# Kernel optimization log

Measured on AMD Instinct MI355X. Metric: run time of the kernel, lower is better.

Reference implementation:

```python
import jax, jax.numpy as jnp
import numpy as np

N, E, F, H, G, C = 50000, 800000, 128, 128, 500, 10
L = 3  # num_conv_layers
EPS = 1e-5


def batch_norm(x, g, b):
    # training-mode BatchNorm1d: biased variance, eps=1e-5
    mu = jnp.mean(x, axis=0)
    var = jnp.var(x, axis=0)
    return (x - mu) * jax.lax.rsqrt(var + EPS) * g + b


def gcn_conv(x, W, bias, src, dst, n):
    # x' = D^{-1/2} (A + I) D^{-1/2} (x W) + bias, edge weights = 1
    xw = x @ W
    loop = jnp.arange(n)
    s = jnp.concatenate([src, loop])  # sources incl. self-loops
    d = jnp.concatenate([dst, loop])  # targets incl. self-loops
    w = jnp.ones(s.shape[0], x.dtype)
    deg = jax.ops.segment_sum(w, s, num_segments=n)
    dinv = jnp.where(deg > 0, jax.lax.rsqrt(deg), 0.0)
    norm = dinv[s] * w * dinv[d]
    msg = xw[s] * norm[:, None]  # gather + scale
    out = jax.ops.segment_sum(msg, d, num_segments=n)  # scatter-add
    return out + bias


def setup_inputs() -> dict:
    key = jax.random.key(0)
    ks = jax.random.split(key, 16)
    x = jax.random.normal(ks[0], (N, F), dtype=jnp.float32)
    edge_index = jax.random.randint(ks[1], (2, E), 0, N, dtype=jnp.int64)
    batch = jnp.sort(jax.random.randint(ks[2], (N,), 0, G, dtype=jnp.int64))
    sF = 1.0 / np.sqrt(F)
    sH = 1.0 / np.sqrt(H)
    return {
        "x": x,
        "edge_index": edge_index,
        "batch": batch,
        "bn_feat_g": jnp.ones((F,), jnp.float32),
        "bn_feat_b": jnp.full((F,), 1e-4, jnp.float32),
        "W_feat": jax.random.normal(ks[3], (F, H), jnp.float32) * sF,
        "bns_conv_g": jnp.ones((L, H), jnp.float32),
        "bns_conv_b": jnp.full((L, H), 1e-4, jnp.float32),
        "W_conv": jax.random.normal(ks[4], (L, H, H), jnp.float32) * sH,
        "b_conv": jnp.zeros((L, H), jnp.float32),
        "bn_fc_g": jnp.ones((H,), jnp.float32),
        "bn_fc_b": jnp.full((H,), 1e-4, jnp.float32),
        "W_lin": jax.random.normal(ks[5], (H, H), jnp.float32) * sH,
        "b_lin": jnp.zeros((H,), jnp.float32),
        "bn_hid_g": jnp.ones((H,), jnp.float32),
        "bn_hid_b": jnp.full((H,), 1e-4, jnp.float32),
        "W_cls": jax.random.normal(ks[6], (H, C), jnp.float32) * sH,
        "b_cls": jnp.zeros((C,), jnp.float32),
    }


def reference(x, edge_index, batch, bn_feat_g, bn_feat_b, W_feat,
              bns_conv_g, bns_conv_b, W_conv, b_conv,
              bn_fc_g, bn_fc_b, W_lin, b_lin,
              bn_hid_g, bn_hid_b, W_cls, b_cls):
    src, dst = edge_index[0], edge_index[1]
    h = batch_norm(x, bn_feat_g, bn_feat_b)
    h = jax.nn.relu(h @ W_feat)  # gfn conv: linear only, no bias/propagation
    for i in range(L):
        h = batch_norm(h, bns_conv_g[i], bns_conv_b[i])
        h = jax.nn.relu(gcn_conv(h, W_conv[i], b_conv[i], src, dst, N))
    h = jax.ops.segment_sum(h, batch, num_segments=G)  # global_add_pool
    h = batch_norm(h, bn_fc_g, bn_fc_b)
    h = jax.nn.relu(h @ W_lin + b_lin)
    h = batch_norm(h, bn_hid_g, bn_hid_b)
    logits = h @ W_cls + b_cls
    return jax.nn.log_softmax(logits, axis=-1)
```

## Files before the change

kernel.cpp:

```cpp
#include <hip/hip_runtime.h>

#define NF 128
#define EPS 1e-5f
#define KELL 64
#define HB 64
#define HRANGE 32768
#define BCAP 5120

typedef unsigned short ushort_t;
typedef unsigned int uint_t;

using bf16x8 = __attribute__((ext_vector_type(8))) short;
using f32x4  = __attribute__((ext_vector_type(4))) float;
using f32x2  = __attribute__((ext_vector_type(2))) float;

static __device__ inline ushort_t f2bf(float f) {
    uint_t u = __float_as_uint(f);
    return (ushort_t)((u + 0x7fffu + ((u >> 16) & 1u)) >> 16);
}


__launch_bounds__(1024)
__global__ void k_bucket(const int* __restrict__ ei, uint_t* __restrict__ gcnt,
                         uint_t* __restrict__ bedge, int E) {
    __shared__ uint_t cnt[256];
    __shared__ uint_t cur[256];
    __shared__ uint_t base[256];
    const int t = threadIdx.x;
    if (t < 256) { cnt[t] = 0; cur[t] = 0; }
    __syncthreads();
    const int chunk = (E + gridDim.x - 1) / gridDim.x;
    const int e0 = blockIdx.x * chunk;
    const int e1 = min(e0 + chunk, E);
    for (int e = e0 + t; e < e1; e += 1024)
        atomicAdd(&cnt[ei[E + e] >> 8], 1);
    __syncthreads();
    if (t < 256) {
        uint_t c = cnt[t];
        base[t] = c ? atomicAdd(&gcnt[t], c) : 0u;
    }
    __syncthreads();
    for (int e = e0 + t; e < e1; e += 1024) {
        int s = ei[e], d = ei[E + e];
        int b = d >> 8;
        uint_t pos = base[b] + atomicAdd(&cur[b], 1);
        if (pos < BCAP)
            bedge[((size_t)b << 12) + ((size_t)b << 10) + pos] =
                ((uint_t)(d & 255) << 16) | (uint_t)s;
    }
}

__global__ void k_hist(const int* __restrict__ ei, uint_t* __restrict__ partial, int E) {
    __shared__ uint_t h2[HRANGE / 2];
    int b = blockIdx.x, t = threadIdx.x;
#pragma unroll
    for (int p = 0; p < 2; ++p) {
        int base = p * HRANGE;
        for (int w = t; w < HRANGE / 2; w += 256) h2[w] = 0;
        __syncthreads();
        for (int e = b * 256 + t; e < E; e += HB * 256) {
            unsigned u = (unsigned)(ei[e] - base);
            if (u < HRANGE)
                atomicAdd(&h2[u >> 1], 1u << ((u & 1) << 4));
        }
        __syncthreads();
        uint_t* dst = partial + ((size_t)(p * HB + b) << 14);
        for (int w = t; w < HRANGE / 2; w += 256) dst[w] = h2[w];
        __syncthreads();
    }
}

__launch_bounds__(256)
__global__ void k_build(const uint_t* __restrict__ gcnt, const uint_t* __restrict__ bedge,
                        const uint_t* __restrict__ hpart, int* __restrict__ ucnt,
                        float* __restrict__ dinv, ushort_t* __restrict__ colx,
                        ushort_t* __restrict__ BbSent, int n) {
    __shared__ ushort_t ell[256][KELL];
    __shared__ uint_t lcnt[256];
    const int b = blockIdx.x, t = threadIdx.x;
    lcnt[t] = 0;
    __syncthreads();
    const int nb = min((int)gcnt[b], BCAP);
    const int node0 = b << 8;
    const uint_t* bsrc = bedge + ((size_t)b << 12) + ((size_t)b << 10);
    for (int e = t; e < nb; e += 256) {
        uint_t pk = bsrc[e];
        int dl = (pk >> 16) & 255;
        uint_t pos = atomicAdd(&lcnt[dl], 1);
        if (pos < KELL - 1) ell[dl][pos] = (ushort_t)(pk & 0xffffu);
    }
    __syncthreads();
    const int i = node0 + t;
    if (i < n) {
        int w = min((int)lcnt[t], KELL - 1);
        ell[t][w] = (ushort_t)i;
        int len = (w + 16) & ~15;
        for (int q = w + 1; q < len; ++q) ell[t][q] = (ushort_t)n;
        ucnt[i] = w;
        int p = i >> 15;
        int u = i & (HRANGE - 1);
        int wd = u >> 1, sh = (u & 1) << 4;
        const uint_t* basep = hpart + ((size_t)(p * HB) << 14) + wd;
        uint_t sum = 0;
#pragma unroll 8
        for (int bb = 0; bb < HB; ++bb) sum += basep[(size_t)bb << 14];
        sum = (sum >> sh) & 0xffffu;
        dinv[i] = rsqrtf((float)sum + 1.0f);
    }
    __syncthreads();
    int nrow = min(n - node0, 256);
    if (nrow > 0) {
        const uint4* src = (const uint4*)&ell[0][0];
        uint4* dst = (uint4*)&colx[(size_t)node0 * KELL];
        int lim = nrow * (KELL * 2 / 16);
        for (int wds = t; wds < lim; wds += 256) dst[wds] = src[wds];
    }
    if (b == 0 && t < 64)
        ((uint_t*)BbSent)[t] = 0;
}


__global__ void bn_stats(const float* __restrict__ h, float* __restrict__ stats, int n) {
    int j = threadIdx.x & 127;
    int half = threadIdx.x >> 7;
    float s = 0.f, q = 0.f;
    for (int r = blockIdx.x * 2 + half; r < n; r += gridDim.x * 2) {
        float v = h[r * NF + j];
        s += v;
        q += v * v;
    }
    __shared__ float ls[256], lq[256];
    ls[threadIdx.x] = s; lq[threadIdx.x] = q;
    __syncthreads();
    if (threadIdx.x < 128) {
        atomicAdd(&stats[j], ls[threadIdx.x] + ls[threadIdx.x + 128]);
        atomicAdd(&stats[NF + j], lq[threadIdx.x] + lq[threadIdx.x + 128]);
    }
}


__global__ void pack_w4(const float* __restrict__ W0, const float* __restrict__ W123,
                        ushort_t* __restrict__ Wp) {
    int gidx = blockIdx.x * 256 + threadIdx.x;
    int mat = gidx >> 11, idx = gidx & 2047;
    const float* W = (mat == 0) ? W0 : (W123 + (size_t)(mat - 1) * NF * NF);
    int lane = idx & 63, ct = (idx >> 6) & 7, kc = idx >> 9;
    int m = lane & 15, q = lane >> 4;
    ushort_t o[8];
#pragma unroll
    for (int j = 0; j < 8; ++j)
        o[j] = f2bf(W[(kc * 32 + q * 8 + j) * NF + ct * 16 + m]);
    *(uint4*)&Wp[(size_t)gidx * 8] = *(uint4*)o;
}


#define HSTRIDE 136

__launch_bounds__(256)
__global__ void gemm_mfma(const float* __restrict__ Hh, const ushort_t* __restrict__ Wp,
                          const float* __restrict__ stats, const float* __restrict__ gW,
                          const float* __restrict__ bB, float inv_n,
                          const float* __restrict__ bias, const float* __restrict__ rowscale,
                          float* __restrict__ out, ushort_t* __restrict__ outb,
                          int nrows, int relu, int obf) {
    __shared__ ushort_t hs[64 * HSTRIDE];
    __shared__ float acs[256];
    const int tid = threadIdx.x;
    const int rb = blockIdx.x * 64;

    if (tid < 128) {
        float mean = stats[tid] * inv_n;
        float var = stats[NF + tid] * inv_n - mean * mean;
        float rstd = rsqrtf(var + EPS);
        float a = gW[tid] * rstd;
        acs[tid] = a;
        acs[NF + tid] = bB[tid] - mean * a;
    }
    __syncthreads();
    const float4* ac4 = (const float4*)acs;

#pragma unroll
    for (int p = 0; p < 8; ++p) {
        int idx = p * 256 + tid;
        int r = idx >> 5, k4 = idx & 31;
        int gr = rb + r;
        float4 v = (gr < nrows) ? *(const float4*)&Hh[(size_t)gr * NF + k4 * 4]
                                : make_float4(0.f, 0.f, 0.f, 0.f);
        float4 a4 = ac4[k4], c4 = ac4[32 + k4];
        ushort_t o[4];
        o[0] = f2bf(fmaf(v.x, a4.x, c4.x));
        o[1] = f2bf(fmaf(v.y, a4.y, c4.y));
        o[2] = f2bf(fmaf(v.z, a4.z, c4.z));
        o[3] = f2bf(fmaf(v.w, a4.w, c4.w));
        *(uint2*)&hs[r * HSTRIDE + k4 * 4] = *(uint2*)o;
    }
    __syncthreads();

    const int wave = tid >> 6, lane = tid & 63;
    const int m = lane & 15, q = lane >> 4;
    const ushort_t* arow = &hs[(wave * 16 + m) * HSTRIDE];

    f32x4 acc[8];
#pragma unroll
    for (int ct = 0; ct < 8; ++ct) acc[ct] = (f32x4){0.f, 0.f, 0.f, 0.f};

#pragma unroll
    for (int kc = 0; kc < 4; ++kc) {
        bf16x8 af = *(const bf16x8*)&arow[kc * 32 + q * 8];
        const ushort_t* wp = Wp + kc * 4096 + lane * 8;
#pragma unroll
        for (int ct = 0; ct < 8; ++ct) {
            bf16x8 bfr = *(const bf16x8*)&wp[ct * 512];
            acc[ct] = __builtin_amdgcn_mfma_f32_16x16x32_bf16(af, bfr, acc[ct], 0, 0, 0);
        }
    }

#pragma unroll
    for (int r = 0; r < 4; ++r) {
        int grow = rb + wave * 16 + q * 4 + r;
        if (grow < nrows) {
            float rs = (obf && rowscale) ? rowscale[grow] : 1.0f;
#pragma unroll
            for (int ct = 0; ct < 8; ++ct) {
                int col = ct * 16 + m;
                float v = acc[ct][r] + (bias ? bias[col] : 0.f);
                if (relu) v = fmaxf(v, 0.f);
                if (obf) outb[(size_t)grow * NF + col] = f2bf(v * rs);
                else     out[(size_t)grow * NF + col] = v;
            }
        }
    }
}


__launch_bounds__(256)
__global__ void gemm_bn(const float* __restrict__ Hh, const float* __restrict__ W,
                        const float* __restrict__ stats, const float* __restrict__ gW,
                        const float* __restrict__ bB, float inv_n,
                        const float* __restrict__ bias,
                        float* __restrict__ out, int nrows, int relu) {
    __shared__ float hsb[64][133];
    __shared__ float acs[256];
    const int tid = threadIdx.x;
    const int tx = tid & 15;
    const int ty = tid >> 4;
    const int rb = blockIdx.x * 64;

    if (tid < 128) {
        float mean = stats[tid] * inv_n;
        float var = stats[NF + tid] * inv_n - mean * mean;
        float rstd = rsqrtf(var + EPS);
        float a = gW[tid] * rstd;
        acs[tid] = a;
        acs[NF + tid] = bB[tid] - mean * a;
    }
    __syncthreads();

#pragma unroll 8
    for (int p = 0; p < 32; ++p) {
        int idx = p * 256 + tid;
        int r = idx >> 7, k = idx & 127;
        int gr = rb + r;
        float v = (gr < nrows) ? Hh[(size_t)gr * NF + k] : 0.f;
        hsb[r][k] = fmaf(v, acs[k], acs[NF + k]);
    }
    __syncthreads();

    float acc[4][8];
#pragma unroll
    for (int i = 0; i < 4; ++i)
#pragma unroll
        for (int j = 0; j < 8; ++j) acc[i][j] = 0.f;

    const int c0 = tx * 4, c1 = 64 + tx * 4;
#pragma unroll 4
    for (int k = 0; k < 128; ++k) {
        const float4 b0 = *(const float4*)&W[k * NF + c0];
        const float4 b1 = *(const float4*)&W[k * NF + c1];
#pragma unroll
        for (int i = 0; i < 4; ++i) {
            float a = hsb[ty * 4 + i][k];
            acc[i][0] = fmaf(a, b0.x, acc[i][0]);
            acc[i][1] = fmaf(a, b0.y, acc[i][1]);
            acc[i][2] = fmaf(a, b0.z, acc[i][2]);
            acc[i][3] = fmaf(a, b0.w, acc[i][3]);
            acc[i][4] = fmaf(a, b1.x, acc[i][4]);
            acc[i][5] = fmaf(a, b1.y, acc[i][5]);
            acc[i][6] = fmaf(a, b1.z, acc[i][6]);
            acc[i][7] = fmaf(a, b1.w, acc[i][7]);
        }
    }

#pragma unroll
    for (int i = 0; i < 4; ++i) {
        int gr = rb + ty * 4 + i;
        if (gr < nrows) {
            float o[8];
#pragma unroll
            for (int j = 0; j < 8; ++j) {
                int c = (j < 4) ? (c0 + j) : (c1 + j - 4);
                float v = acc[i][j] + (bias ? bias[c] : 0.f);
                o[j] = relu ? fmaxf(v, 0.f) : v;
            }
            *(float4*)&out[(size_t)gr * NF + c0] = make_float4(o[0], o[1], o[2], o[3]);
            *(float4*)&out[(size_t)gr * NF + c1] = make_float4(o[4], o[5], o[6], o[7]);
        }
    }
}


#define ACC2(u, j) { f32x2 t;                                   \
    t.x = __uint_as_float((u) << 16);                           \
    t.y = __uint_as_float((u) & 0xffff0000u);                   \
    acc2[j] += t; }
#define ACC8(q) { ACC2(q.x, 0) ACC2(q.y, 1) ACC2(q.z, 2) ACC2(q.w, 3) }

__launch_bounds__(256)
__global__ void k_aggregate_bf(const ushort_t* __restrict__ xwb, const int* __restrict__ ucnt,
                               const ushort_t* __restrict__ colx, const float* __restrict__ dinv,
                               const float* __restrict__ bias, float* __restrict__ out, int n) {
    int node = blockIdx.x * 16 + (threadIdx.x >> 4);
    int lane = threadIdx.x & 15;
    if (node >= n) return;
    const uint4* __restrict__ xq = (const uint4*)xwb;
    f32x2 acc2[4];
#pragma unroll
    for (int j = 0; j < 4; ++j) acc2[j] = (f32x2){0.f, 0.f};
    int dc = min(ucnt[node], KELL - 1);
    int len = (dc + 16) & ~15;
    int e0 = node * KELL;
    for (int e = e0; e < e0 + len; e += 16) {
        uint4 ia = *(const uint4*)&colx[e];
        uint4 ib = *(const uint4*)&colx[e + 8];
        int i0 = ia.x & 0xffff, i1 = ia.x >> 16;
        int i2 = ia.y & 0xffff, i3 = ia.y >> 16;
        int i4 = ia.z & 0xffff, i5 = ia.z >> 16;
        int i6 = ia.w & 0xffff, i7 = ia.w >> 16;
        int i8 = ib.x & 0xffff, i9 = ib.x >> 16;
        int iA = ib.y & 0xffff, iB = ib.y >> 16;
        int iC = ib.z & 0xffff, iD = ib.z >> 16;
        int iE = ib.w & 0xffff, iF = ib.w >> 16;
        uint4 q0 = xq[(size_t)i0 * 16 + lane];
        uint4 q1 = xq[(size_t)i1 * 16 + lane];
        uint4 q2 = xq[(size_t)i2 * 16 + lane];
        uint4 q3 = xq[(size_t)i3 * 16 + lane];
        uint4 q4 = xq[(size_t)i4 * 16 + lane];
        uint4 q5 = xq[(size_t)i5 * 16 + lane];
        uint4 q6 = xq[(size_t)i6 * 16 + lane];
        uint4 q7 = xq[(size_t)i7 * 16 + lane];
        uint4 q8 = xq[(size_t)i8 * 16 + lane];
        uint4 q9 = xq[(size_t)i9 * 16 + lane];
        uint4 qA = xq[(size_t)iA * 16 + lane];
        uint4 qB = xq[(size_t)iB * 16 + lane];
        uint4 qC = xq[(size_t)iC * 16 + lane];
        uint4 qD = xq[(size_t)iD * 16 + lane];
        uint4 qE = xq[(size_t)iE * 16 + lane];
        uint4 qF = xq[(size_t)iF * 16 + lane];
        ACC8(q0) ACC8(q1) ACC8(q2) ACC8(q3)
        ACC8(q4) ACC8(q5) ACC8(q6) ACC8(q7)
        ACC8(q8) ACC8(q9) ACC8(qA) ACC8(qB)
        ACC8(qC) ACC8(qD) ACC8(qE) ACC8(qF)
    }
    float di = dinv[node];
    float4 b0 = *(const float4*)&bias[lane * 8];
    float4 b1 = *(const float4*)&bias[lane * 8 + 4];
    float4 o0, o1;
    o0.x = fmaxf(fmaf(di, acc2[0].x, b0.x), 0.f);
    o0.y = fmaxf(fmaf(di, acc2[0].y, b0.y), 0.f);
    o0.z = fmaxf(fmaf(di, acc2[1].x, b0.z), 0.f);
    o0.w = fmaxf(fmaf(di, acc2[1].y, b0.w), 0.f);
    o1.x = fmaxf(fmaf(di, acc2[2].x, b1.x), 0.f);
    o1.y = fmaxf(fmaf(di, acc2[2].y, b1.y), 0.f);
    o1.z = fmaxf(fmaf(di, acc2[3].x, b1.z), 0.f);
    o1.w = fmaxf(fmaf(di, acc2[3].y, b1.w), 0.f);
    *(float4*)&out[(size_t)node * NF + lane * 8] = o0;
    *(float4*)&out[(size_t)node * NF + lane * 8 + 4] = o1;
}


__global__ void k_pool(const float* __restrict__ h, const int* __restrict__ batch,
                       float* __restrict__ pooled, float* __restrict__ stats, int n) {
    int g = blockIdx.x;
    int t = threadIdx.x;
    int lo = 0, hi = n;
    while (lo < hi) { int m = (lo + hi) >> 1; if (batch[m] < g) lo = m + 1; else hi = m; }
    int start = lo;
    lo = start; hi = n;
    while (lo < hi) { int m = (lo + hi) >> 1; if (batch[m] < g + 1) lo = m + 1; else hi = m; }
    int end = lo;
    float a0 = 0.f, a1 = 0.f, a2 = 0.f, a3 = 0.f;
    int r = start;
    for (; r + 4 <= end; r += 4) {
        a0 += h[(size_t)r * NF + t];
        a1 += h[(size_t)(r + 1) * NF + t];
        a2 += h[(size_t)(r + 2) * NF + t];
        a3 += h[(size_t)(r + 3) * NF + t];
    }
    for (; r < end; ++r) a0 += h[(size_t)r * NF + t];
    float val = (a0 + a1) + (a2 + a3);
    pooled[g * NF + t] = val;
    atomicAdd(&stats[t], val);
    atomicAdd(&stats[NF + t], val * val);
}


__global__ void k_cls(const float* __restrict__ h, const float* __restrict__ stats,
                      const float* __restrict__ gW, const float* __restrict__ bB,
                      float inv_n, const float* __restrict__ Wc,
                      const float* __restrict__ bc, float* __restrict__ out, int C_) {
    __shared__ float hr[128];
    __shared__ float lg[16];
    __shared__ float lse_s;
    int r = blockIdx.x, t = threadIdx.x;
#pragma unroll
    for (int half = 0; half < 2; ++half) {
        int j = t + half * 64;
        float mean = stats[j] * inv_n;
        float var = stats[NF + j] * inv_n - mean * mean;
        float rstd = rsqrtf(var + EPS);
        float a = gW[j] * rstd;
        float c = bB[j] - mean * a;
        hr[j] = fmaf(h[r * NF + j], a, c);
    }
    __syncthreads();
    if (t < C_) {
        float s = bc[t];
        for (int k = 0; k < 128; ++k) s = fmaf(hr[k], Wc[k * C_ + t], s);
        lg[t] = s;
    }
    __syncthreads();
    if (t == 0) {
        float m = -1e30f;
        for (int c = 0; c < C_; ++c) m = fmaxf(m, lg[c]);
        float se = 0.f;
        for (int c = 0; c < C_; ++c) se += expf(lg[c] - m);
        lse_s = m + logf(se);
    }
    __syncthreads();
    if (t < C_) out[r * C_ + t] = lg[t] - lse_s;
}


extern "C" void kernel_launch(void* const* d_in, const int* in_sizes, int n_in,
                              void* d_out, int out_size, void* d_ws, size_t ws_size,
                              hipStream_t stream) {
    const float* x          = (const float*)d_in[0];
    const int*   ei         = (const int*)d_in[1];
    const int*   batch      = (const int*)d_in[2];
    const float* bn_feat_g  = (const float*)d_in[3];
    const float* bn_feat_b  = (const float*)d_in[4];
    const float* W_feat     = (const float*)d_in[5];
    const float* bns_conv_g = (const float*)d_in[6];
    const float* bns_conv_b = (const float*)d_in[7];
    const float* W_conv     = (const float*)d_in[8];
    const float* b_conv     = (const float*)d_in[9];
    const float* bn_fc_g    = (const float*)d_in[10];
    const float* bn_fc_b    = (const float*)d_in[11];
    const float* W_lin      = (const float*)d_in[12];
    const float* b_lin      = (const float*)d_in[13];
    const float* bn_hid_g   = (const float*)d_in[14];
    const float* bn_hid_b   = (const float*)d_in[15];
    const float* W_cls      = (const float*)d_in[16];
    const float* b_cls      = (const float*)d_in[17];
    float* outp = (float*)d_out;

    const int N_ = in_sizes[2];
    const int E_ = in_sizes[1] / 2;
    const int C_ = 10;
    const int G_ = out_size / C_;
    const int NBUCK = (N_ + 255) >> 8;

    char* wsp = (char*)d_ws;
    auto alloc = [&](size_t bytes) {
        void* p = (void*)wsp;
        wsp += (bytes + 255) & ~(size_t)255;
        return p;
    };
    uint_t*   gcnt   = (uint_t*)alloc(256 * 4);
    float*    statsA = (float*)alloc(6 * 256 * 4);
    float*    A      = (float*)alloc((size_t)N_ * NF * 4);
    ushort_t* Bb     = (ushort_t*)alloc((size_t)(N_ + 1) * NF * 2);
    float*    dinv   = (float*)alloc((size_t)N_ * 4);
    int*      ucnt   = (int*)alloc((size_t)N_ * 4);
    uint_t*   bedge  = (uint_t*)alloc((size_t)256 * BCAP * 4);
    ushort_t* colx   = (ushort_t*)alloc((size_t)N_ * KELL * 2);
    uint_t*   hpart  = (uint_t*)alloc((size_t)2 * HB * (HRANGE / 2) * 4);
    ushort_t* Wp     = (ushort_t*)alloc((size_t)4 * NF * NF * 2);
    float*    pooled = (float*)alloc((size_t)G_ * NF * 4);
    float*    y2     = (float*)alloc((size_t)G_ * NF * 4);

    float* st_x  = statsA;
    float* st_f  = statsA + 256;
    float* st_a1 = statsA + 512;
    float* st_a2 = statsA + 768;
    float* st_pl = statsA + 1024;
    float* st_y2 = statsA + 1280;

    int nb_g = (N_ + 63) / 64;

    hipMemsetAsync(gcnt, 0, 1024 + 6 * 256 * 4, stream);

    k_bucket<<<256, 1024, 0, stream>>>(ei, gcnt, bedge, E_);
    k_hist<<<HB, 256, 0, stream>>>(ei, hpart, E_);
    k_build<<<NBUCK, 256, 0, stream>>>(gcnt, bedge, hpart, ucnt, dinv, colx,
                                       Bb + (size_t)N_ * NF, N_);

    pack_w4<<<32, 256, 0, stream>>>(W_feat, W_conv, Wp);

    bn_stats<<<512, 256, 0, stream>>>(x, st_x, N_);
    gemm_mfma<<<nb_g, 256, 0, stream>>>(x, Wp, st_x, bn_feat_g, bn_feat_b, 1.0f / N_,
                                        nullptr, nullptr, A, nullptr, N_, 1, 0);
    bn_stats<<<512, 256, 0, stream>>>(A, st_f, N_);

    float* st_in[3] = {st_f, st_a1, st_a2};
    float* st_out[3] = {st_a1, st_a2, nullptr};
    for (int l = 0; l < 3; ++l) {
        gemm_mfma<<<nb_g, 256, 0, stream>>>(A, Wp + (size_t)(l + 1) * NF * NF,
                                            st_in[l], bns_conv_g + l * NF, bns_conv_b + l * NF,
                                            1.0f / N_, nullptr, dinv, nullptr, Bb, N_, 0, 1);
        k_aggregate_bf<<<(N_ + 15) / 16, 256, 0, stream>>>(Bb, ucnt, colx, dinv,
                                                           b_conv + l * NF, A, N_);
        if (st_out[l])
            bn_stats<<<512, 256, 0, stream>>>(A, st_out[l], N_);
    }

    k_pool<<<G_, 128, 0, stream>>>(A, batch, pooled, st_pl, N_);

    gemm_bn<<<(G_ + 63) / 64, 256, 0, stream>>>(pooled, W_lin, st_pl, bn_fc_g, bn_fc_b,
                                                1.0f / G_, b_lin, y2, G_, 1);
    bn_stats<<<512, 256, 0, stream>>>(y2, st_y2, G_);

    k_cls<<<G_, 64, 0, stream>>>(y2, st_y2, bn_hid_g, bn_hid_b, 1.0f / G_,
                                 W_cls, b_cls, outp, C_);
}
```

Measured before the change: 479.3 us.

## Fuse BN statistics into GEMM/aggregate epilogues and merge prep kernels

Computes the column sum and sum-of-squares for batch norm inside the epilogues of the GEMM, aggregation and small GEMM kernels, which removes four separate bn_stats passes over the activations. The bucket, histogram and weight-packing kernels become one launch split by block index. The ELL padding granularity drops from 16 to 8 entries, which cuts wasted gathers, and the aggregate kernel now uses 1024-thread blocks. In exchange it adds shared and global atomics plus block syncs in the epilogues, and the per-thread float accumulation order changes.

Result: no change. 486.0 us (+1.4%).

```diff
diff --git a/kernel.cpp b/kernel.cpp
--- a/kernel.cpp
+++ b/kernel.cpp
@@ -21,52 +21,70 @@
 
 
 __launch_bounds__(1024)
-__global__ void k_bucket(const int* __restrict__ ei, uint_t* __restrict__ gcnt,
-                         uint_t* __restrict__ bedge, int E) {
-    __shared__ uint_t cnt[256];
-    __shared__ uint_t cur[256];
-    __shared__ uint_t base[256];
+__global__ void k_prep(const int* __restrict__ ei, uint_t* __restrict__ gcnt,
+                       uint_t* __restrict__ bedge, uint_t* __restrict__ hpart,
+                       const float* __restrict__ W0, const float* __restrict__ W123,
+                       ushort_t* __restrict__ Wp, int E) {
+    __shared__ union {
+        struct { uint_t cnt[256]; uint_t cur[256]; uint_t base[256]; } bk;
+        uint_t h2[HRANGE / 2];
+    } sh;
+    const int blk = blockIdx.x;
     const int t = threadIdx.x;
-    if (t < 256) { cnt[t] = 0; cur[t] = 0; }
-    __syncthreads();
-    const int chunk = (E + gridDim.x - 1) / gridDim.x;
-    const int e0 = blockIdx.x * chunk;
-    const int e1 = min(e0 + chunk, E);
-    for (int e = e0 + t; e < e1; e += 1024)
-        atomicAdd(&cnt[ei[E + e] >> 8], 1);
-    __syncthreads();
-    if (t < 256) {
-        uint_t c = cnt[t];
-        base[t] = c ? atomicAdd(&gcnt[t], c) : 0u;
-    }
-    __syncthreads();
-    for (int e = e0 + t; e < e1; e += 1024) {
-        int s = ei[e], d = ei[E + e];
-        int b = d >> 8;
-        uint_t pos = base[b] + atomicAdd(&cur[b], 1);
-        if (pos < BCAP)
-            bedge[((size_t)b << 12) + ((size_t)b << 10) + pos] =
-                ((uint_t)(d & 255) << 16) | (uint_t)s;
-    }
-}
-
-__global__ void k_hist(const int* __restrict__ ei, uint_t* __restrict__ partial, int E) {
-    __shared__ uint_t h2[HRANGE / 2];
-    int b = blockIdx.x, t = threadIdx.x;
-#pragma unroll
-    for (int p = 0; p < 2; ++p) {
-        int base = p * HRANGE;
-        for (int w = t; w < HRANGE / 2; w += 256) h2[w] = 0;
-        __syncthreads();
-        for (int e = b * 256 + t; e < E; e += HB * 256) {
-            unsigned u = (unsigned)(ei[e] - base);
-            if (u < HRANGE)
-                atomicAdd(&h2[u >> 1], 1u << ((u & 1) << 4));
-        }
-        __syncthreads();
-        uint_t* dst = partial + ((size_t)(p * HB + b) << 14);
-        for (int w = t; w < HRANGE / 2; w += 256) dst[w] = h2[w];
-        __syncthreads();
+
+    if (blk < 256) {
+        if (t < 256) { sh.bk.cnt[t] = 0; sh.bk.cur[t] = 0; }
+        __syncthreads();
+        const int chunk = (E + 255) / 256;
+        const int e0 = blk * chunk;
+        const int e1 = min(e0 + chunk, E);
+        for (int e = e0 + t; e < e1; e += 1024)
+            atomicAdd(&sh.bk.cnt[ei[E + e] >> 8], 1);
+        __syncthreads();
+        if (t < 256) {
+            uint_t c = sh.bk.cnt[t];
+            sh.bk.base[t] = c ? atomicAdd(&gcnt[t], c) : 0u;
+        }
+        __syncthreads();
+        for (int e = e0 + t; e < e1; e += 1024) {
+            int s = ei[e], d = ei[E + e];
+            int b = d >> 8;
+            uint_t pos = sh.bk.base[b] + atomicAdd(&sh.bk.cur[b], 1);
+            if (pos < BCAP)
+                bedge[((size_t)b << 12) + ((size_t)b << 10) + pos] =
+                    ((uint_t)(d & 255) << 16) | (uint_t)s;
+        }
+    } else if (blk < 320) {
+        const int b = blk - 256;
+#pragma unroll
+        for (int p = 0; p < 2; ++p) {
+            int base = p * HRANGE;
+            for (int w = t; w < HRANGE / 2; w += 1024) sh.h2[w] = 0;
+            __syncthreads();
+            for (int e = b * 1024 + t; e < E; e += HB * 1024) {
+                unsigned u = (unsigned)(ei[e] - base);
+                if (u < HRANGE)
+                    atomicAdd(&sh.h2[u >> 1], 1u << ((u & 1) << 4));
+            }
+            __syncthreads();
+            uint_t* dst = hpart + ((size_t)(p * HB + b) << 14);
+            for (int w = t; w < HRANGE / 2; w += 1024) dst[w] = sh.h2[w];
+            __syncthreads();
+        }
+    } else {
+#pragma unroll
+        for (int kk = 0; kk < 4; ++kk) {
+            int gidx = (blk - 320) * 4096 + kk * 1024 + t;
+            int mat = gidx >> 11, idx = gidx & 2047;
+            const float* W = (mat == 0) ? W0 : (W123 + (size_t)(mat - 1) * NF * NF);
+            int lane = idx & 63, ct = (idx >> 6) & 7, kc = idx >> 9;
+            int m = lane & 15, q = lane >> 4;
+            ushort_t o[8];
+#pragma unroll
+            for (int j = 0; j < 8; ++j)
+                o[j] = f2bf(W[(kc * 32 + q * 8 + j) * NF + ct * 16 + m]);
+            *(uint4*)&Wp[(size_t)gidx * 8] = *(uint4*)o;
+        }
     }
 }
 
@@ -94,7 +112,7 @@
     if (i < n) {
         int w = min((int)lcnt[t], KELL - 1);
         ell[t][w] = (ushort_t)i;
-        int len = (w + 16) & ~15;
+        int len = (w + 8) & ~7;
         for (int q = w + 1; q < len; ++q) ell[t][q] = (ushort_t)n;
         ucnt[i] = w;
         int p = i >> 15;
@@ -139,21 +157,6 @@
 }
 
 
-__global__ void pack_w4(const float* __restrict__ W0, const float* __restrict__ W123,
-                        ushort_t* __restrict__ Wp) {
-    int gidx = blockIdx.x * 256 + threadIdx.x;
-    int mat = gidx >> 11, idx = gidx & 2047;
-    const float* W = (mat == 0) ? W0 : (W123 + (size_t)(mat - 1) * NF * NF);
-    int lane = idx & 63, ct = (idx >> 6) & 7, kc = idx >> 9;
-    int m = lane & 15, q = lane >> 4;
-    ushort_t o[8];
-#pragma unroll
-    for (int j = 0; j < 8; ++j)
-        o[j] = f2bf(W[(kc * 32 + q * 8 + j) * NF + ct * 16 + m]);
-    *(uint4*)&Wp[(size_t)gidx * 8] = *(uint4*)o;
-}
-
-
 #define HSTRIDE 136
 
 __launch_bounds__(256)
@@ -162,9 +165,11 @@
                           const float* __restrict__ bB, float inv_n,
                           const float* __restrict__ bias, const float* __restrict__ rowscale,
                           float* __restrict__ out, ushort_t* __restrict__ outb,
+                          float* __restrict__ statsOut,
                           int nrows, int relu, int obf) {
     __shared__ ushort_t hs[64 * HSTRIDE];
     __shared__ float acs[256];
+    __shared__ float cs[128], cq[128];
     const int tid = threadIdx.x;
     const int rb = blockIdx.x * 64;
 
@@ -175,6 +180,7 @@
         float a = gW[tid] * rstd;
         acs[tid] = a;
         acs[NF + tid] = bB[tid] - mean * a;
+        cs[tid] = 0.f; cq[tid] = 0.f;
     }
     __syncthreads();
     const float4* ac4 = (const float4*)acs;
@@ -215,19 +221,37 @@
         }
     }
 
+    int grows[4]; float rsv[4]; bool gv[4];
 #pragma unroll
     for (int r = 0; r < 4; ++r) {
-        int grow = rb + wave * 16 + q * 4 + r;
-        if (grow < nrows) {
-            float rs = (obf && rowscale) ? rowscale[grow] : 1.0f;
-#pragma unroll
-            for (int ct = 0; ct < 8; ++ct) {
-                int col = ct * 16 + m;
-                float v = acc[ct][r] + (bias ? bias[col] : 0.f);
+        grows[r] = rb + wave * 16 + q * 4 + r;
+        gv[r] = grows[r] < nrows;
+        rsv[r] = (obf && rowscale && gv[r]) ? rowscale[grows[r]] : 1.0f;
+    }
+#pragma unroll
+    for (int ct = 0; ct < 8; ++ct) {
+        int col = ct * 16 + m;
+        float bcol = bias ? bias[col] : 0.f;
+        float s = 0.f, qq = 0.f;
+#pragma unroll
+        for (int r = 0; r < 4; ++r) {
+            if (gv[r]) {
+                float v = acc[ct][r] + bcol;
                 if (relu) v = fmaxf(v, 0.f);
-                if (obf) outb[(size_t)grow * NF + col] = f2bf(v * rs);
-                else     out[(size_t)grow * NF + col] = v;
+                if (obf) outb[(size_t)grows[r] * NF + col] = f2bf(v * rsv[r]);
+                else {
+                    out[(size_t)grows[r] * NF + col] = v;
+                    s += v; qq += v * v;
+                }
             }
+        }
+        if (statsOut) { atomicAdd(&cs[col], s); atomicAdd(&cq[col], qq); }
+    }
+    if (statsOut) {
+        __syncthreads();
+        if (tid < 128) {
+            atomicAdd(&statsOut[tid], cs[tid]);
+            atomicAdd(&statsOut[NF + tid], cq[tid]);
         }
     }
 }
@@ -238,9 +262,11 @@
                         const float* __restrict__ stats, const float* __restrict__ gW,
                         const float* __restrict__ bB, float inv_n,
                         const float* __restrict__ bias,
-                        float* __restrict__ out, int nrows, int relu) {
+                        float* __restrict__ out, float* __restrict__ statsOut,
+                        int nrows, int relu) {
     __shared__ float hsb[64][133];
     __shared__ float acs[256];
+    __shared__ float cs[128], cq[128];
     const int tid = threadIdx.x;
     const int tx = tid & 15;
     const int ty = tid >> 4;
@@ -253,6 +279,7 @@
         float a = gW[tid] * rstd;
         acs[tid] = a;
         acs[NF + tid] = bB[tid] - mean * a;
+        cs[tid] = 0.f; cq[tid] = 0.f;
     }
     __syncthreads();
 
@@ -291,6 +318,9 @@
         }
     }
 
+    float scol[8], qcol[8];
+#pragma unroll
+    for (int j = 0; j < 8; ++j) { scol[j] = 0.f; qcol[j] = 0.f; }
 #pragma unroll
     for (int i = 0; i < 4; ++i) {
         int gr = rb + ty * 4 + i;
@@ -301,80 +331,109 @@
                 int c = (j < 4) ? (c0 + j) : (c1 + j - 4);
                 float v = acc[i][j] + (bias ? bias[c] : 0.f);
                 o[j] = relu ? fmaxf(v, 0.f) : v;
+                scol[j] += o[j]; qcol[j] += o[j] * o[j];
             }
             *(float4*)&out[(size_t)gr * NF + c0] = make_float4(o[0], o[1], o[2], o[3]);
             *(float4*)&out[(size_t)gr * NF + c1] = make_float4(o[4], o[5], o[6], o[7]);
         }
     }
-}
-
-
-#define ACC2(u, j) { f32x2 t;                                   \
-    t.x = __uint_as_float((u) << 16);                           \
-    t.y = __uint_as_float((u) & 0xffff0000u);                   \
-    acc2[j] += t; }
+    if (statsOut) {
+#pragma unroll
+        for (int j = 0; j < 8; ++j) {
+            int c = (j < 4) ? (c0 + j) : (c1 + j - 4);
+            atomicAdd(&cs[c], scol[j]);
+            atomicAdd(&cq[c], qcol[j]);
+        }
+        __syncthreads();
+        if (tid < 128) {
+            atomicAdd(&statsOut[tid], cs[tid]);
+            atomicAdd(&statsOut[NF + tid], cq[tid]);
+        }
+    }
+}
+
+
+#define ACC2(u, j) { f32x2 t_;                                  \
+    t_.x = __uint_as_float((u) << 16);                          \
+    t_.y = __uint_as_float((u) & 0xffff0000u);                  \
+    acc2[j] += t_; }
 #define ACC8(q) { ACC2(q.x, 0) ACC2(q.y, 1) ACC2(q.z, 2) ACC2(q.w, 3) }
 
-__launch_bounds__(256)
+__launch_bounds__(1024)
 __global__ void k_aggregate_bf(const ushort_t* __restrict__ xwb, const int* __restrict__ ucnt,
                                const ushort_t* __restrict__ colx, const float* __restrict__ dinv,
-                               const float* __restrict__ bias, float* __restrict__ out, int n) {
-    int node = blockIdx.x * 16 + (threadIdx.x >> 4);
-    int lane = threadIdx.x & 15;
-    if (node >= n) return;
+                               const float* __restrict__ bias, float* __restrict__ out,
+                               float* __restrict__ statsOut, int n) {
+    __shared__ float cs[128], cq[128];
+    const int tid = threadIdx.x;
+    const int node = blockIdx.x * 64 + (tid >> 4);
+    const int lane = tid & 15;
+    if (statsOut && tid < 128) { cs[tid] = 0.f; cq[tid] = 0.f; }
     const uint4* __restrict__ xq = (const uint4*)xwb;
     f32x2 acc2[4];
 #pragma unroll
     for (int j = 0; j < 4; ++j) acc2[j] = (f32x2){0.f, 0.f};
-    int dc = min(ucnt[node], KELL - 1);
-    int len = (dc + 16) & ~15;
-    int e0 = node * KELL;
-    for (int e = e0; e < e0 + len; e += 16) {
-        uint4 ia = *(const uint4*)&colx[e];
-        uint4 ib = *(const uint4*)&colx[e + 8];
-        int i0 = ia.x & 0xffff, i1 = ia.x >> 16;
-        int i2 = ia.y & 0xffff, i3 = ia.y >> 16;
-        int i4 = ia.z & 0xffff, i5 = ia.z >> 16;
-        int i6 = ia.w & 0xffff, i7 = ia.w >> 16;
-        int i8 = ib.x & 0xffff, i9 = ib.x >> 16;
-        int iA = ib.y & 0xffff, iB = ib.y >> 16;
-        int iC = ib.z & 0xffff, iD = ib.z >> 16;
-        int iE = ib.w & 0xffff, iF = ib.w >> 16;
-        uint4 q0 = xq[(size_t)i0 * 16 + lane];
-        uint4 q1 = xq[(size_t)i1 * 16 + lane];
-        uint4 q2 = xq[(size_t)i2 * 16 + lane];
-        uint4 q3 = xq[(size_t)i3 * 16 + lane];
-        uint4 q4 = xq[(size_t)i4 * 16 + lane];
-        uint4 q5 = xq[(size_t)i5 * 16 + lane];
-        uint4 q6 = xq[(size_t)i6 * 16 + lane];
-        uint4 q7 = xq[(size_t)i7 * 16 + lane];
-        uint4 q8 = xq[(size_t)i8 * 16 + lane];
-        uint4 q9 = xq[(size_t)i9 * 16 + lane];
-        uint4 qA = xq[(size_t)iA * 16 + lane];
-        uint4 qB = xq[(size_t)iB * 16 + lane];
-        uint4 qC = xq[(size_t)iC * 16 + lane];
-        uint4 qD = xq[(size_t)iD * 16 + lane];
-        uint4 qE = xq[(size_t)iE * 16 + lane];
-        uint4 qF = xq[(size_t)iF * 16 + lane];
-        ACC8(q0) ACC8(q1) ACC8(q2) ACC8(q3)
-        ACC8(q4) ACC8(q5) ACC8(q6) ACC8(q7)
-        ACC8(q8) ACC8(q9) ACC8(qA) ACC8(qB)
-        ACC8(qC) ACC8(qD) ACC8(qE) ACC8(qF)
-    }
-    float di = dinv[node];
-    float4 b0 = *(const float4*)&bias[lane * 8];
-    float4 b1 = *(const float4*)&bias[lane * 8 + 4];
-    float4 o0, o1;
-    o0.x = fmaxf(fmaf(di, acc2[0].x, b0.x), 0.f);
-    o0.y = fmaxf(fmaf(di, acc2[0].y, b0.y), 0.f);
-    o0.z = fmaxf(fmaf(di, acc2[1].x, b0.z), 0.f);
-    o0.w = fmaxf(fmaf(di, acc2[1].y, b0.w), 0.f);
-    o1.x = fmaxf(fmaf(di, acc2[2].x, b1.x), 0.f);
-    o1.y = fmaxf(fmaf(di, acc2[2].y, b1.y), 0.f);
-    o1.z = fmaxf(fmaf(di, acc2[3].x, b1.z), 0.f);
-    o1.w = fmaxf(fmaf(di, acc2[3].y, b1.w), 0.f);
-    *(float4*)&out[(size_t)node * NF + lane * 8] = o0;
-    *(float4*)&out[(size_t)node * NF + lane * 8 + 4] = o1;
+    const bool valid = node < n;
+    if (valid) {
+        int dc = min(ucnt[node], KELL - 1);
+        int len = (dc + 8) & ~7;
+        int e0 = node * KELL;
+        for (int e = e0; e < e0 + len; e += 8) {
+            uint4 ia = *(const uint4*)&colx[e];
+            int i0 = ia.x & 0xffff, i1 = ia.x >> 16;
+            int i2 = ia.y & 0xffff, i3 = ia.y >> 16;
+            int i4 = ia.z & 0xffff, i5 = ia.z >> 16;
+            int i6 = ia.w & 0xffff, i7 = ia.w >> 16;
+            uint4 q0 = xq[(size_t)i0 * 16 + lane];
+            uint4 q1 = xq[(size_t)i1 * 16 + lane];
+            uint4 q2 = xq[(size_t)i2 * 16 + lane];
+            uint4 q3 = xq[(size_t)i3 * 16 + lane];
+            uint4 q4 = xq[(size_t)i4 * 16 + lane];
+            uint4 q5 = xq[(size_t)i5 * 16 + lane];
+            uint4 q6 = xq[(size_t)i6 * 16 + lane];
+            uint4 q7 = xq[(size_t)i7 * 16 + lane];
+            ACC8(q0) ACC8(q1) ACC8(q2) ACC8(q3)
+            ACC8(q4) ACC8(q5) ACC8(q6) ACC8(q7)
+        }
+    }
+    float vals[8];
+#pragma unroll
+    for (int j = 0; j < 8; ++j) vals[j] = 0.f;
+    if (valid) {
+        float di = dinv[node];
+        float4 b0 = *(const float4*)&bias[lane * 8];
+        float4 b1 = *(const float4*)&bias[lane * 8 + 4];
+        vals[0] = fmaxf(fmaf(di, acc2[0].x, b0.x), 0.f);
+        vals[1] = fmaxf(fmaf(di, acc2[0].y, b0.y), 0.f);
+        vals[2] = fmaxf(fmaf(di, acc2[1].x, b0.z), 0.f);
+        vals[3] = fmaxf(fmaf(di, acc2[1].y, b0.w), 0.f);
+        vals[4] = fmaxf(fmaf(di, acc2[2].x, b1.x), 0.f);
+        vals[5] = fmaxf(fmaf(di, acc2[2].y, b1.y), 0.f);
+        vals[6] = fmaxf(fmaf(di, acc2[3].x, b1.z), 0.f);
+        vals[7] = fmaxf(fmaf(di, acc2[3].y, b1.w), 0.f);
+        *(float4*)&out[(size_t)node * NF + lane * 8] =
+            make_float4(vals[0], vals[1], vals[2], vals[3]);
+        *(float4*)&out[(size_t)node * NF + lane * 8 + 4] =
+            make_float4(vals[4], vals[5], vals[6], vals[7]);
+    }
+    if (statsOut) {
+        __syncthreads();
+#pragma unroll
+        for (int j = 0; j < 8; ++j) {
+            float v = vals[j], qv = vals[j] * vals[j];
+            v += __shfl_xor(v, 16); qv += __shfl_xor(qv, 16);
+            v += __shfl_xor(v, 32); qv += __shfl_xor(qv, 32);
+            if ((tid & 63) < 16) {
+                atomicAdd(&cs[lane * 8 + j], v);
+                atomicAdd(&cq[lane * 8 + j], qv);
+            }
+        }
+        __syncthreads();
+        if (tid < 128) {
+            atomicAdd(&statsOut[tid], cs[tid]);
+            atomicAdd(&statsOut[NF + tid], cq[tid]);
+        }
+    }
 }
 
 
@@ -497,38 +556,33 @@
     float* st_y2 = statsA + 1280;
 
     int nb_g = (N_ + 63) / 64;
+    int nb_ag = (N_ + 63) / 64;
 
     hipMemsetAsync(gcnt, 0, 1024 + 6 * 256 * 4, stream);
 
-    k_bucket<<<256, 1024, 0, stream>>>(ei, gcnt, bedge, E_);
-    k_hist<<<HB, 256, 0, stream>>>(ei, hpart, E_);
+    k_prep<<<322, 1024, 0, stream>>>(ei, gcnt, bedge, hpart, W_feat, W_conv, Wp, E_);
     k_build<<<NBUCK, 256, 0, stream>>>(gcnt, bedge, hpart, ucnt, dinv, colx,
                                        Bb + (size_t)N_ * NF, N_);
 
-    pack_w4<<<32, 256, 0, stream>>>(W_feat, W_conv, Wp);
-
     bn_stats<<<512, 256, 0, stream>>>(x, st_x, N_);
     gemm_mfma<<<nb_g, 256, 0, stream>>>(x, Wp, st_x, bn_feat_g, bn_feat_b, 1.0f / N_,
-                                        nullptr, nullptr, A, nullptr, N_, 1, 0);
-    bn_stats<<<512, 256, 0, stream>>>(A, st_f, N_);
+                                        nullptr, nullptr, A, nullptr, st_f, N_, 1, 0);
 
     float* st_in[3] = {st_f, st_a1, st_a2};
     float* st_out[3] = {st_a1, st_a2, nullptr};
     for (int l = 0; l < 3; ++l) {
         gemm_mfma<<<nb_g, 256, 0, stream>>>(A, Wp + (size_t)(l + 1) * NF * NF,
                                             st_in[l], bns_conv_g + l * NF, bns_conv_b + l * NF,
-                                            1.0f / N_, nullptr, dinv, nullptr, Bb, N_, 0, 1);
-        k_aggregate_bf<<<(N_ + 15) / 16, 256, 0, stream>>>(Bb, ucnt, colx, dinv,
-                                                           b_conv + l * NF, A, N_);
-        if (st_out[l])
-            bn_stats<<<512, 256, 0, stream>>>(A, st_out[l], N_);
+                                            1.0f / N_, nullptr, dinv, nullptr, Bb, nullptr,
+                                            N_, 0, 1);
+        k_aggregate_bf<<<nb_ag, 1024, 0, stream>>>(Bb, ucnt, colx, dinv,
+                                                   b_conv + l * NF, A, st_out[l], N_);
     }
 
     k_pool<<<G_, 128, 0, stream>>>(A, batch, pooled, st_pl, N_);
 
     gemm_bn<<<(G_ + 63) / 64, 256, 0, stream>>>(pooled, W_lin, st_pl, bn_fc_g, bn_fc_b,
-                                                1.0f / G_, b_lin, y2, G_, 1);
-    bn_stats<<<512, 256, 0, stream>>>(y2, st_y2, G_);
+                                                1.0f / G_, b_lin, y2, st_y2, G_, 1);
 
     k_cls<<<G_, 64, 0, stream>>>(y2, st_y2, bn_hid_g, bn_hid_b, 1.0f / G_,
                                  W_cls, b_cls, outp, C_);
```
